# Kernel tuning notes

Measured on AMD Instinct MI355X. Metric: run time of the kernel, lower is better.

## Reference

```python
import jax, jax.numpy as jnp
import numpy as np

# Detector / Siddon constants (from init_kwargs)
H, W = 200, 200
DELX, DELY = 1.5, 1.5
NXV, NYV, NZV = 256, 256, 256  # voxel counts
EPS = 1e-8


def setup_inputs() -> dict:
    key = jax.random.key(0)
    kvol, = jax.random.split(key, 1)
    volume = jax.random.uniform(kvol, (NXV, NYV, NZV), dtype=jnp.float32)  # CT intensities
    spacing = jnp.ones((3,), jnp.float32)                                  # 1mm isotropic
    sdr = jnp.array([300.0], jnp.float32)                                  # source-to-detector radius
    rotations = jnp.array([[0.5, -0.2, 0.3]], jnp.float32)                 # theta, phi, gamma
    translations = jnp.array([[128.0, 128.0, 128.0]], jnp.float32)         # volume center (bx,by,bz)
    return {"volume": volume, "spacing": spacing, "sdr": sdr,
            "rotations": rotations, "translations": translations}


def _rotation_matrix(rotations):
    # R = Rz(theta) @ Ry(phi) @ Rx(gamma), batched
    theta, phi, gamma = rotations[:, 0], rotations[:, 1], rotations[:, 2]
    ct, st = jnp.cos(theta), jnp.sin(theta)
    cp, sp = jnp.cos(phi), jnp.sin(phi)
    cg, sg = jnp.cos(gamma), jnp.sin(gamma)
    z = jnp.zeros_like(theta)
    o = jnp.ones_like(theta)
    Rz = jnp.stack([ct, -st, z, st, ct, z, z, z, o], -1).reshape(-1, 3, 3)
    Ry = jnp.stack([cp, z, sp, z, o, z, -sp, z, cp], -1).reshape(-1, 3, 3)
    Rx = jnp.stack([o, z, z, z, cg, -sg, z, sg, cg], -1).reshape(-1, 3, 3)
    return Rz @ Ry @ Rx


def _make_xrays(sdr, rotations, translations):
    # Detector.make_xrays: source on column 0 of sdr*R, detector center opposite,
    # detector plane spanned by unit columns 1 and 2.
    R = _rotation_matrix(rotations)                 # (b,3,3), orthonormal columns
    source = sdr[:, None] * R[..., 0]               # (b,3)
    center = -source
    basis = jnp.stack([R[..., 1], R[..., 2]], 1)    # (b,2,3)
    source = source + translations
    center = center + translations
    t = (jnp.arange(-(H // 2), H // 2, dtype=jnp.float32) + 1.0) * DELX
    s = (jnp.arange(-(W // 2), W // 2, dtype=jnp.float32) + 1.0) * DELY
    coefs = jnp.stack(jnp.meshgrid(t, s, indexing="ij"), -1).reshape(-1, 2)  # (H*W,2) == cartesian_prod(t,s)
    target = jnp.einsum("bcd,nc->bnd", basis, coefs) + center[:, None, :]    # (b,n,3)
    return source[:, None, :], target               # (b,1,3), (b,n,3)


def reference(volume, spacing, sdr, rotations, translations):
    source, target = _make_xrays(sdr, rotations, translations)
    vol = jnp.flip(volume, 0)                       # Siddon flips axis 0
    nx, ny, nz = vol.shape
    sdd = target - source + EPS                     # (b,n,3) ray directions

    # Alphas at every axis-aligned plane intersection: P = (nx+1)+(ny+1)+(nz+1)
    alphas = jnp.concatenate(
        [(jnp.arange(n + 1, dtype=jnp.float32) * spacing[i] - source[..., i:i + 1]) / sdd[..., i:i + 1]
         for i, n in enumerate((nx, ny, nz))], axis=-1)          # (b,n,P)

    # Entry/exit alphas of the volume bounding box
    extent = jnp.asarray([nx, ny, nz], jnp.float32) * spacing
    a0 = (0.0 - source) / sdd
    a1 = (extent - source) / sdd
    amin = jnp.max(jnp.minimum(a0, a1), -1, keepdims=True)       # (b,n,1)
    amax = jnp.min(jnp.maximum(a0, a1), -1, keepdims=True)

    # Out-of-range alphas -> sentinel amax (sorts to the end, contributes zero step;
    # equivalent to the original's NaN + nansum handling)
    valid = (alphas >= amin) & (alphas <= amax)
    alphas = jnp.sort(jnp.where(valid, alphas, amax), axis=-1)

    mid = 0.5 * (alphas[..., :-1] + alphas[..., 1:])             # (b,n,P-1)
    step = jnp.diff(alphas, axis=-1)

    # Midpoint positions -> voxel indices (trunc, clamped in-bounds)
    xyz = source[:, :, None, :] + mid[..., None] * sdd[:, :, None, :]  # (b,n,P-1,3)
    idx = jnp.trunc(xyz / spacing).astype(jnp.int32)
    ix = jnp.clip(idx[..., 0], 0, nx - 1)
    iy = jnp.clip(idx[..., 1], 0, ny - 1)
    iz = jnp.clip(idx[..., 2], 0, nz - 1)
    voxels = vol[ix, iy, iz]                                     # gather, (b,n,P-1)

    drr = jnp.sum(voxels * step, -1) * jnp.linalg.norm(sdd, axis=-1)
    return drr.reshape(-1, H, W)
```

## Files before the change

### kernel.cpp

```cpp
#include <hip/hip_runtime.h>

#define H_ 200
#define W_ 200
#define DELX_ 1.5f
#define DELY_ 1.5f
#define NXV_ 256
#define NYV_ 256
#define NZV_ 256
#define EPS_ 1e-8f
#define NSEG 16
#define SEGS_PER_THR 2
#define TILE_R 4
#define TILE_C 16
#define TROWS (H_ / TILE_R)
#define TCOLS ((W_ + TILE_C - 1) / TILE_C)
#define TILES_PER_IMG (TROWS * TCOLS)
#define G_ 8
#define MAXG 10

__device__ __forceinline__ float alpha_mul(float k, float sp, float src, float inv_sdd) {
    return (k * sp - src) * inv_sdd;
}

#define MARCH(OFF, STP)                                                       \
    _Pragma("unroll")                                                         \
    for (int u = 0; u < G_; ++u) {                                            \
        float an = fminf(axv, fminf(ayv, azv));                               \
        bool ok = (an <= aend);                                               \
        STP[u] = ok ? (an - a_cur) : 0.0f;                                    \
        OFF[u] = off_cur;                                                     \
        a_cur = an;                                                           \
        bool upd = (an < aend);                                               \
        bool cx = (axv == an), cy = (ayv == an), cz = (azv == an);            \
        kx = cx ? kx + dkx : kx;                                              \
        ky = cy ? ky + dky : ky;                                              \
        kz = cz ? kz + dkz : kz;                                              \
        off_cur += ((cx && upd) ? doffx : 0)                                  \
                 + ((cy && upd) ? doffy : 0)                                  \
                 + ((cz && upd) ? doffz : 0);                                 \
        axv = alpha_mul(kx, spx, sx, inv_dx);   \
        ayv = alpha_mul(ky, spy, sy, inv_dy);                                 \
        azv = alpha_mul(kz, spz, sz, inv_dz);                                 \
    }

__global__ void __launch_bounds__(512, 6)
drr_tile(const float* __restrict__ vol,
         const float* __restrict__ spacing,
         const float* __restrict__ sdr,
         const float* __restrict__ rot,
         const float* __restrict__ trans,
         float* __restrict__ out) {
    const int t = threadIdx.x;
    const int pixLocal = t & 63;
    const int segBase = t >> 6;

    const int b    = blockIdx.x / TILES_PER_IMG;
    const int rem  = blockIdx.x % TILES_PER_IMG;
    const int ty   = rem / TCOLS;
    const int tx   = rem % TCOLS;
    const int i = ty * TILE_R + (pixLocal >> 4);
    const int j = tx * TILE_C + (pixLocal & 15);

    const float theta = rot[b * 3 + 0], phi = rot[b * 3 + 1], gamma = rot[b * 3 + 2];
    const float ct = cosf(theta), st = sinf(theta);
    const float cp = cosf(phi),   sp = sinf(phi);
    const float cg = cosf(gamma), sg = sinf(gamma);
    const float r00 = ct * cp,                r10 = st * cp,                r20 = -sp;
    const float r01 = ct * sp * sg - st * cg, r11 = st * sp * sg + ct * cg, r21 = cp * sg;
    const float r02 = ct * sp * cg + st * sg, r12 = st * sp * cg - ct * sg, r22 = cp * cg;

    const float sd = sdr[b];
    const float tx_ = trans[b * 3 + 0], ty_ = trans[b * 3 + 1], tz_ = trans[b * 3 + 2];
    const float sx = sd * r00 + tx_, sy = sd * r10 + ty_, sz = sd * r20 + tz_;
    const float cxx = -sd * r00 + tx_, cyy = -sd * r10 + ty_, czz = -sd * r20 + tz_;

    const float tco = ((float)(i - H_ / 2) + 1.0f) * DELX_;
    const float sco = ((float)(j - W_ / 2) + 1.0f) * DELY_;
    const float gx = r01 * tco + r02 * sco + cxx;
    const float gy = r11 * tco + r12 * sco + cyy;
    const float gz = r21 * tco + r22 * sco + czz;

    const float dx = gx - sx + EPS_;
    const float dy = gy - sy + EPS_;
    const float dz = gz - sz + EPS_;

    const float spx = spacing[0], spy = spacing[1], spz = spacing[2];
    const float inv_spx = 1.0f / spx, inv_spy = 1.0f / spy, inv_spz = 1.0f / spz;
    const float inv_dx = 1.0f / dx, inv_dy = 1.0f / dy, inv_dz = 1.0f / dz;

    const float a0x = alpha_mul(0.f, spx, sx, inv_dx), a1x = alpha_mul((float)NXV_, spx, sx, inv_dx);
    const float a0y = alpha_mul(0.f, spy, sy, inv_dy), a1y = alpha_mul((float)NYV_, spy, sy, inv_dy);
    const float a0z = alpha_mul(0.f, spz, sz, inv_dz), a1z = alpha_mul((float)NZV_, spz, sz, inv_dz);

    const float amin = fmaxf(fmaxf(fminf(a0x, a1x), fminf(a0y, a1y)), fminf(a0z, a1z));
    const float amax = fminf(fminf(fmaxf(a0x, a1x), fmaxf(a0y, a1y)), fmaxf(a0z, a1z));

    const float norm = sqrtf(dx * dx + dy * dy + dz * dz);

    const int doffy0 = NZV_, doffz0 = 1;

    __shared__ float red[NSEG * 64];

    #pragma unroll 1
    for (int s2 = 0; s2 < SEGS_PER_THR; ++s2) {
        const int seg = segBase + (s2 << 3);

        const float klo = (float)(seg * (NXV_ / NSEG));
        const float khi = (float)((seg + 1) * (NXV_ / NSEG));
        const float aA = alpha_mul(klo, spx, sx, inv_dx);
        const float aB = alpha_mul(khi, spx, sx, inv_dx);
        const float start = fmaxf(amin, fminf(aA, aB));
        const float aend  = fminf(amax, fmaxf(aA, aB));

        float acc = 0.0f;
        if (start < aend) {
            float kx, ky, kz, axv, ayv, azv, dkx, dky, dkz;
            {
                float kf = (start * dx + sx) * inv_spx;
                if (dx > 0.f) { dkx = 1.f;  kx = floorf(kf) + 1.f; }
                else          { dkx = -1.f; kx = ceilf(kf) - 1.f; }
                axv = alpha_mul(kx, spx, sx, inv_dx);
            }
            {
                float kf = (start * dy + sy) * inv_spy;
                if (dy > 0.f) { dky = 1.f;  ky = floorf(kf) + 1.f; }
                else          { dky = -1.f; ky = ceilf(kf) - 1.f; }
                ayv = alpha_mul(ky, spy, sy, inv_dy);
            }
            {
                float kf = (start * dz + sz) * inv_spz;
                if (dz > 0.f) { dkz = 1.f;  kz = floorf(kf) + 1.f; }
                else          { dkz = -1.f; kz = ceilf(kf) - 1.f; }
                azv = alpha_mul(kz, spz, sz, inv_dz);
            }

            int off_cur;
            {
                float an0 = fminf(axv, fminf(ayv, azv));
                float midv = 0.5f * (start + an0);
                int ix = (int)((sx + midv * dx) * inv_spx);
                int iy = (int)((sy + midv * dy) * inv_spy);
                int iz = (int)((sz + midv * dz) * inv_spz);
                ix = min(max(ix, 0), NXV_ - 1);
                iy = min(max(iy, 0), NYV_ - 1);
                iz = min(max(iz, 0), NZV_ - 1);
                off_cur = ((NXV_ - 1 - ix) * NYV_ + iy) * NZV_ + iz;
            }
            const int doffx = (dkx > 0.f) ? -(NYV_ * NZV_) : (NYV_ * NZV_);
            const int doffy = (dky > 0.f) ? doffy0 : -doffy0;
            const int doffz = (dkz > 0.f) ? doffz0 : -doffz0;

            float a_cur = start;
            int   off[G_];
            float stp[G_], v[G_];

            #pragma unroll 1
            for (int g = 0; g < MAXG; ++g) {
                MARCH(off, stp);
                #pragma unroll
                for (int u = 0; u < G_; ++u) v[u] = vol[off[u]];
                #pragma unroll
                for (int u = 0; u < G_; ++u) acc += v[u] * stp[u];
                if (__all(a_cur > aend)) break;
            }
        }
        red[(s2 << 9) + t] = acc * norm;
    }

    __syncthreads();
    if (t < 64) {
        const int ii = ty * TILE_R + (t >> 4);
        const int jj = tx * TILE_C + (t & 15);
        if (jj < W_) {
            float sLo = 0.0f, sHi = 0.0f;
            #pragma unroll
            for (int k = 0; k < 8; ++k) sLo += red[t + k * 64];
            #pragma unroll
            for (int k = 0; k < 8; ++k) sHi += red[512 + t + k * 64];
            out[b * (H_ * W_) + ii * W_ + jj] = sLo + sHi;
        }
    }
}

extern "C" void kernel_launch(void* const* d_in, const int* in_sizes, int n_in,
                              void* d_out, int out_size, void* d_ws, size_t ws_size,
                              hipStream_t stream) {
    const float* vol     = (const float*)d_in[0];
    const float* spacing = (const float*)d_in[1];
    const float* sdr     = (const float*)d_in[2];
    const float* rot     = (const float*)d_in[3];
    const float* trans   = (const float*)d_in[4];
    float* out = (float*)d_out;

    const int B = in_sizes[2];
    drr_tile<<<B * TILES_PER_IMG, 512, 0, stream>>>(vol, spacing, sdr, rot, trans, out);
}
```

Before: 121.2 us.

## Interleave two ray segments per thread and remap blocks across XCDs

Each thread now marches its two segments at the same time instead of one after the other. Per step it issues 4 gathers for each segment, so 8 loads are in flight per iteration from two independent chains, and both chains share a single early-exit vote. Blocks are also remapped so that consecutive tiles land on the same XCD, which is meant to improve L2 locality of the volume gathers. The cost is more live registers per thread, and a wave keeps iterating until its slowest segment on either chain has finished.

```diff
diff --git a/kernel.cpp b/kernel.cpp
--- a/kernel.cpp
+++ b/kernel.cpp
@@ -9,38 +9,78 @@
 #define NZV_ 256
 #define EPS_ 1e-8f
 #define NSEG 16
-#define SEGS_PER_THR 2
 #define TILE_R 4
 #define TILE_C 16
 #define TROWS (H_ / TILE_R)
 #define TCOLS ((W_ + TILE_C - 1) / TILE_C)
 #define TILES_PER_IMG (TROWS * TCOLS)
-#define G_ 8
-#define MAXG 10
+#define G4 4
+#define MAXG 20
 
 __device__ __forceinline__ float alpha_mul(float k, float sp, float src, float inv_sdd) {
     return (k * sp - src) * inv_sdd;
 }
 
-#define MARCH(OFF, STP)                                                       \
-    _Pragma("unroll")                                                         \
-    for (int u = 0; u < G_; ++u) {                                            \
-        float an = fminf(axv, fminf(ayv, azv));                               \
-        bool ok = (an <= aend);                                               \
-        STP[u] = ok ? (an - a_cur) : 0.0f;                                    \
-        OFF[u] = off_cur;                                                     \
-        a_cur = an;                                                           \
-        bool upd = (an < aend);                                               \
-        bool cx = (axv == an), cy = (ayv == an), cz = (azv == an);            \
-        kx = cx ? kx + dkx : kx;                                              \
-        ky = cy ? ky + dky : ky;                                              \
-        kz = cz ? kz + dkz : kz;                                              \
-        off_cur += ((cx && upd) ? doffx : 0)                                  \
-                 + ((cy && upd) ? doffy : 0)                                  \
-                 + ((cz && upd) ? doffz : 0);                                 \
-        axv = alpha_mul(kx, spx, sx, inv_dx);   \
-        ayv = alpha_mul(ky, spy, sy, inv_dy);                                 \
-        azv = alpha_mul(kz, spz, sz, inv_dz);                                 \
+#define STEPC(N, u)                                                           \
+    {                                                                         \
+        float an = fminf(axv##N, fminf(ayv##N, azv##N));                      \
+        bool ok = (an <= aend##N);                                            \
+        stp##N[u] = ok ? (an - a_cur##N) : 0.0f;                              \
+        off##N[u] = off_cur##N;                                               \
+        a_cur##N = an;                                                        \
+        bool upd = (an < aend##N);                                            \
+        bool cx = (axv##N == an), cy = (ayv##N == an), cz = (azv##N == an);   \
+        kx##N = cx ? kx##N + dkx : kx##N;                                     \
+        ky##N = cy ? ky##N + dky : ky##N;                                     \
+        kz##N = cz ? kz##N + dkz : kz##N;                                     \
+        off_cur##N += ((cx && upd) ? doffx : 0)                               \
+                    + ((cy && upd) ? doffy : 0)                               \
+                    + ((cz && upd) ? doffz : 0);                              \
+        axv##N = alpha_mul(kx##N, spx, sx, inv_dx);                           \
+        ayv##N = alpha_mul(ky##N, spy, sy, inv_dy);                           \
+        azv##N = alpha_mul(kz##N, spz, sz, inv_dz);                           \
+    }
+
+#define INIT_CH(N, SEGV)                                                      \
+    float start##N, aend##N, kx##N, ky##N, kz##N, axv##N, ayv##N, azv##N;     \
+    float a_cur##N, acc##N = 0.0f;                                            \
+    int off_cur##N;                                                           \
+    {                                                                         \
+        const float klo = (float)((SEGV) * (NXV_ / NSEG));                    \
+        const float khi = (float)(((SEGV) + 1) * (NXV_ / NSEG));              \
+        const float aA = alpha_mul(klo, spx, sx, inv_dx);                     \
+        const float aB = alpha_mul(khi, spx, sx, inv_dx);                     \
+        start##N = fmaxf(amin, fminf(aA, aB));                                \
+        aend##N  = fminf(amax, fmaxf(aA, aB));                                \
+        const bool live = start##N < aend##N;                                 \
+        {                                                                     \
+            float kf = (start##N * dx + sx) * inv_spx;                        \
+            kx##N = (dx > 0.f) ? floorf(kf) + 1.f : ceilf(kf) - 1.f;          \
+            axv##N = alpha_mul(kx##N, spx, sx, inv_dx);                       \
+        }                                                                     \
+        {                                                                     \
+            float kf = (start##N * dy + sy) * inv_spy;                        \
+            ky##N = (dy > 0.f) ? floorf(kf) + 1.f : ceilf(kf) - 1.f;          \
+            ayv##N = alpha_mul(ky##N, spy, sy, inv_dy);                       \
+        }                                                                     \
+        {                                                                     \
+            float kf = (start##N * dz + sz) * inv_spz;                        \
+            kz##N = (dz > 0.f) ? floorf(kf) + 1.f : ceilf(kf) - 1.f;          \
+            azv##N = alpha_mul(kz##N, spz, sz, inv_dz);                       \
+        }                                                                     \
+        {                                                                     \
+            float an0 = fminf(axv##N, fminf(ayv##N, azv##N));                 \
+            float midv = 0.5f * (start##N + an0);                             \
+            int ix = (int)((sx + midv * dx) * inv_spx);      \
+            int iy = (int)((sy + midv * dy) * inv_spy);                       \
+            int iz = (int)((sz + midv * dz) * inv_spz);                       \
+            ix = min(max(ix, 0), NXV_ - 1);                                   \
+            iy = min(max(iy, 0), NYV_ - 1);                                   \
+            iz = min(max(iz, 0), NZV_ - 1);                                   \
+            off_cur##N = ((NXV_ - 1 - ix) * NYV_ + iy) * NZV_ + iz;           \
+        }                                                                     \
+        a_cur##N = start##N;                                                  \
+        if (!live) aend##N = -3.0e38f;                                        \
     }
 
 __global__ void __launch_bounds__(512, 6)
@@ -50,12 +90,18 @@
          const float* __restrict__ rot,
          const float* __restrict__ trans,
          float* __restrict__ out) {
+    const int nwg = gridDim.x;
+    const int q8 = nwg >> 3, r8 = nwg & 7;
+    const int xcd = blockIdx.x & 7;
+    const int sub = blockIdx.x >> 3;
+    const int wg = (xcd < r8 ? xcd * (q8 + 1) : r8 * (q8 + 1) + (xcd - r8) * q8) + sub;
+
     const int t = threadIdx.x;
     const int pixLocal = t & 63;
-    const int segBase = t >> 6;
-
-    const int b    = blockIdx.x / TILES_PER_IMG;
-    const int rem  = blockIdx.x % TILES_PER_IMG;
+    const int seg1 = t >> 6;
+
+    const int b    = wg / TILES_PER_IMG;
+    const int rem  = wg % TILES_PER_IMG;
     const int ty   = rem / TCOLS;
     const int tx   = rem % TCOLS;
     const int i = ty * TILE_R + (pixLocal >> 4);
@@ -97,76 +143,36 @@
 
     const float norm = sqrtf(dx * dx + dy * dy + dz * dz);
 
-    const int doffy0 = NZV_, doffz0 = 1;
+    const float dkx = (dx > 0.f) ? 1.f : -1.f;
+    const float dky = (dy > 0.f) ? 1.f : -1.f;
+    const float dkz = (dz > 0.f) ? 1.f : -1.f;
+    const int doffx = (dx > 0.f) ? -(NYV_ * NZV_) : (NYV_ * NZV_);
+    const int doffy = (dy > 0.f) ? NZV_ : -NZV_;
+    const int doffz = (dz > 0.f) ? 1 : -1;
+
+    INIT_CH(1, seg1)
+    INIT_CH(2, seg1 + 8)
+
+    #pragma unroll 1
+    for (int g = 0; g < MAXG; ++g) {
+        int   off1[G4], off2[G4];
+        float stp1[G4], stp2[G4], v1[G4], v2[G4];
+        STEPC(1, 0) STEPC(2, 0)
+        STEPC(1, 1) STEPC(2, 1)
+        STEPC(1, 2) STEPC(2, 2)
+        STEPC(1, 3) STEPC(2, 3)
+        #pragma unroll
+        for (int u = 0; u < G4; ++u) { v1[u] = vol[off1[u]]; v2[u] = vol[off2[u]]; }
+        #pragma unroll
+        for (int u = 0; u < G4; ++u) { acc1 += v1[u] * stp1[u]; }
+        #pragma unroll
+        for (int u = 0; u < G4; ++u) { acc2 += v2[u] * stp2[u]; }
+        if (__all((a_cur1 > aend1) && (a_cur2 > aend2))) break;
+    }
 
     __shared__ float red[NSEG * 64];
-
-    #pragma unroll 1
-    for (int s2 = 0; s2 < SEGS_PER_THR; ++s2) {
-        const int seg = segBase + (s2 << 3);
-
-        const float klo = (float)(seg * (NXV_ / NSEG));
-        const float khi = (float)((seg + 1) * (NXV_ / NSEG));
-        const float aA = alpha_mul(klo, spx, sx, inv_dx);
-        const float aB = alpha_mul(khi, spx, sx, inv_dx);
-        const float start = fmaxf(amin, fminf(aA, aB));
-        const float aend  = fminf(amax, fmaxf(aA, aB));
-
-        float acc = 0.0f;
-        if (start < aend) {
-            float kx, ky, kz, axv, ayv, azv, dkx, dky, dkz;
-            {
-                float kf = (start * dx + sx) * inv_spx;
-                if (dx > 0.f) { dkx = 1.f;  kx = floorf(kf) + 1.f; }
-                else          { dkx = -1.f; kx = ceilf(kf) - 1.f; }
-                axv = alpha_mul(kx, spx, sx, inv_dx);
-            }
-            {
-                float kf = (start * dy + sy) * inv_spy;
-                if (dy > 0.f) { dky = 1.f;  ky = floorf(kf) + 1.f; }
-                else          { dky = -1.f; ky = ceilf(kf) - 1.f; }
-                ayv = alpha_mul(ky, spy, sy, inv_dy);
-            }
-            {
-                float kf = (start * dz + sz) * inv_spz;
-                if (dz > 0.f) { dkz = 1.f;  kz = floorf(kf) + 1.f; }
-                else          { dkz = -1.f; kz = ceilf(kf) - 1.f; }
-                azv = alpha_mul(kz, spz, sz, inv_dz);
-            }
-
-            int off_cur;
-            {
-                float an0 = fminf(axv, fminf(ayv, azv));
-                float midv = 0.5f * (start + an0);
-                int ix = (int)((sx + midv * dx) * inv_spx);
-                int iy = (int)((sy + midv * dy) * inv_spy);
-                int iz = (int)((sz + midv * dz) * inv_spz);
-                ix = min(max(ix, 0), NXV_ - 1);
-                iy = min(max(iy, 0), NYV_ - 1);
-                iz = min(max(iz, 0), NZV_ - 1);
-                off_cur = ((NXV_ - 1 - ix) * NYV_ + iy) * NZV_ + iz;
-            }
-            const int doffx = (dkx > 0.f) ? -(NYV_ * NZV_) : (NYV_ * NZV_);
-            const int doffy = (dky > 0.f) ? doffy0 : -doffy0;
-            const int doffz = (dkz > 0.f) ? doffz0 : -doffz0;
-
-            float a_cur = start;
-            int   off[G_];
-            float stp[G_], v[G_];
-
-            #pragma unroll 1
-            for (int g = 0; g < MAXG; ++g) {
-                MARCH(off, stp);
-                #pragma unroll
-                for (int u = 0; u < G_; ++u) v[u] = vol[off[u]];
-                #pragma unroll
-                for (int u = 0; u < G_; ++u) acc += v[u] * stp[u];
-                if (__all(a_cur > aend)) break;
-            }
-        }
-        red[(s2 << 9) + t] = acc * norm;
-    }
-
+    red[seg1 * 64 + pixLocal]       = acc1 * norm;
+    red[(seg1 + 8) * 64 + pixLocal] = acc2 * norm;
     __syncthreads();
     if (t < 64) {
         const int ii = ty * TILE_R + (t >> 4);
@@ -174,9 +180,9 @@
         if (jj < W_) {
             float sLo = 0.0f, sHi = 0.0f;
             #pragma unroll
-            for (int k = 0; k < 8; ++k) sLo += red[t + k * 64];
+            for (int k = 0; k < 8; ++k) sLo += red[k * 64 + t];
             #pragma unroll
-            for (int k = 0; k < 8; ++k) sHi += red[512 + t + k * 64];
+            for (int k = 8; k < 16; ++k) sHi += red[k * 64 + t];
             out[b * (H_ * W_) + ii * W_ + jj] = sLo + sHi;
         }
     }
```

Result: no change. 122.4 us (+1.0%).
